# Performance work log

Measured on AMD Instinct MI355X. Metric: run time of the kernel, lower is better.

## Reference

```python
import jax, jax.numpy as jnp
import numpy as np

B, T, N, F = 8, 60, 400, 64
UNITS = 64
TIME_LEN = 12  # temporal conv kernel length
NEG = 1e16


def setup_inputs() -> dict:
    key = jax.random.key(0)
    ks = jax.random.split(key, 20)
    s = 0.05  # weight scale
    # sparse binary adjacency (k-hop support) with self-loops
    probs = jax.random.uniform(ks[0], (N, N))
    A = jnp.maximum((probs < 0.03).astype(jnp.float32), jnp.eye(N, dtype=jnp.float32))
    x = jax.random.normal(ks[1], (B, T, N, F), dtype=jnp.float32)
    inp = {
        'x': x,
        'A': A,
        # DynamicGC params
        'dgc_W1': jax.random.normal(ks[2], (N, N)) * s,
        'dgc_W2': jax.random.normal(ks[3], (F, N)) * s,
        'dgc_W3': jax.random.normal(ks[4], (F, UNITS)) * s,
        'dgc_b1': jax.random.normal(ks[5], (N,)) * s,
        'dgc_b2': jnp.zeros((UNITS,), jnp.float32),
        # TemporalAttention params (built on (T, N, UNITS))
        'ta_W1': jax.random.normal(ks[6], (N, 1)) * s,
        'ta_W2': jax.random.normal(ks[7], (UNITS, N)) * s,
        'ta_W3': jax.random.normal(ks[8], (UNITS, 1)) * s,
        'ta_Ve': jax.random.normal(ks[9], (T, T)) * s,
        'ta_be': jnp.zeros((T, T), jnp.float32),
        # temporal convs, kernel (TIME_LEN, 1), padding SAME, HWIO layout
        'tconv_k': jax.random.normal(ks[10], (TIME_LEN, 1, UNITS, UNITS)) * s,
        'tconv_b': jnp.zeros((UNITS,), jnp.float32),
        'rconv_k': jax.random.normal(ks[11], (TIME_LEN, 1, F, UNITS)) * s,
        'rconv_b': jnp.zeros((UNITS,), jnp.float32),
    }
    return inp


def _conv2d_same(x, k, b):
    # x: (B, T, N, Cin) NHWC, k: (TIME_LEN, 1, Cin, Cout) HWIO
    y = jax.lax.conv_general_dilated(
        x, k, window_strides=(1, 1), padding='SAME',
        dimension_numbers=('NHWC', 'HWIO', 'NHWC'))
    return y + b


def reference(x, A, dgc_W1, dgc_W2, dgc_W3, dgc_b1, dgc_b2,
              ta_W1, ta_W2, ta_W3, ta_Ve, ta_be,
              tconv_k, tconv_b, rconv_k, rconv_b):
    # ---- DynamicGC (TimeDistributed over T) ----
    AW = A * dgc_W1                                  # (N, N)
    # feature[b,t,m,f] = sum_n x[b,t,n,f] * AW[n,m]
    feat = jnp.einsum('btnf,nm->btmf', x, AW)
    dense = jnp.einsum('btmf,fj->btmj', feat, dgc_W2) + dgc_b1  # (B,T,N,N)
    logits = dense - NEG * (1.0 - A)
    attn = jax.nn.softmax(logits, axis=-1)           # (B,T,N,N)
    nodef = jnp.einsum('btmn,btnf->btmf', attn, x)   # (B,T,N,F)
    y = jnp.einsum('btnf,fu->btnu', nodef, dgc_W3) + dgc_b2  # (B,T,N,UNITS), linear activation

    # ---- TemporalAttention ----
    # lhs[b,t,n] = sum_f (sum_m y[b,t,m,f] * W1[m,0]) * W2[f,n]
    r1 = jnp.einsum('btnf,n->btf', y, ta_W1[:, 0])   # (B,T,UNITS)
    lhs = jnp.einsum('btf,fn->btn', r1, ta_W2)       # (B,T,N)
    rhs = jnp.einsum('btnf,f->btn', y, ta_W3[:, 0])  # (B,T,N), then transposed in contraction
    product = jnp.einsum('btn,bsn->bts', lhs, rhs)   # (B,T,T)
    E = jnp.einsum('jk,bkl->bjl', ta_Ve, jax.nn.sigmoid(product + ta_be))
    kernel = jax.nn.softmax(E, axis=-2)              # softmax over axis -2, (B,T,T)
    # conv[b,m,n,f] = sum_t y[b,t,n,f] * kernel[b,t,m]
    ta_out = jnp.einsum('btnf,btm->bmnf', y, kernel)  # (B,T,N,UNITS)

    # ---- temporal convs + residual + softplus ----
    tc = _conv2d_same(ta_out, tconv_k, tconv_b)
    res = _conv2d_same(x, rconv_k, rconv_b)
    return jax.nn.softplus(res + tc)
```

## Files before the change

kernel.cpp:

```cpp
#include <hip/hip_runtime.h>
#include <hip/hip_bf16.h>

typedef __attribute__((ext_vector_type(8))) short short8;
typedef __attribute__((ext_vector_type(4))) short short4_t;
typedef __attribute__((ext_vector_type(4))) float f32x4;

union P8u { unsigned char b[8]; long v; };

static __device__ __forceinline__ short f2b(float f) {
    union { float f; unsigned u; } v; v.f = f;
    unsigned r = v.u + 0x7FFFu + ((v.u >> 16) & 1u);
    return (short)(r >> 16);
}
static __device__ __forceinline__ unsigned char f2fp8(float f) {
    return (unsigned char)(__builtin_amdgcn_cvt_pk_fp8_f32(f, f, 0, false) & 0xff);
}

__global__ __launch_bounds__(256) void prep_w(
    const float* __restrict__ A, const float* __restrict__ W1,
    const float* __restrict__ W2, const float* __restrict__ W3,
    short* __restrict__ AWF, short* __restrict__ W2F,
    short* __restrict__ W3F, unsigned char* __restrict__ Ab2)
{
    int t = blockIdx.x * 256 + threadIdx.x;
    if (t < 422 * 64) {
        int tile = t >> 6, lane = t & 63, lm = lane & 15, quad = lane >> 4;
        short8 o;
        if (tile < 364) {
            int kt = tile % 13, g = tile / 13;
            int m = g * 16 + lm;
#pragma unroll
            for (int j = 0; j < 8; ++j) {
                int n = kt * 32 + quad * 8 + j;
                float v = (m < 400 && n < 400) ? A[n * 400 + m] * W1[n * 400 + m] : 0.f;
                o[j] = f2b(v);
            }
            *(short8*)(AWF + tile * 512 + lane * 8) = o;
        } else if (tile < 414) {
            int t2 = tile - 364;
            int kh = t2 & 1, jt = t2 >> 1;
            int jc = jt * 16 + lm;
#pragma unroll
            for (int j = 0; j < 8; ++j) {
                int f = kh * 32 + quad * 8 + j;
                o[j] = f2b(W2[f * 400 + jc]);
            }
            *(short8*)(W2F + t2 * 512 + lane * 8) = o;
        } else {
            int t3 = tile - 414;
            int kh = t3 & 1, ut = t3 >> 1;
            int u = ut * 16 + lm;
#pragma unroll
            for (int j = 0; j < 8; ++j) {
                int f = kh * 32 + quad * 8 + j;
                o[j] = f2b(W3[f * 64 + u]);
            }
            *(short8*)(W3F + t3 * 512 + lane * 8) = o;
        }
    } else {
        int o = t - 27008;
        if (o < 448 * 448) {
            int m = o / 448, j = o - m * 448;
            Ab2[o] = (m < 400 && j < 400 && A[m * 400 + j] != 0.f) ? 1 : 0;
        }
    }
}

__global__ __launch_bounds__(256) void prep_xt(
    const float* __restrict__ x, short* __restrict__ xF,
    unsigned char* __restrict__ xF8)
{
    int bt = blockIdx.x / 13, kt = blockIdx.x % 13;
    int tid = threadIdx.x, lane = tid & 63, ft = tid >> 6;
    int lm = lane & 15, quad = lane >> 4;
    const float* xs = x + (size_t)bt * 25600;
    int tile = kt * 4 + ft;
    int f = ft * 16 + lm;
    short8 ob; P8u p8;
#pragma unroll
    for (int j = 0; j < 8; ++j) {
        int n = kt * 32 + quad * 8 + j;
        float v = (n < 400) ? xs[(size_t)n * 64 + f] : 0.f;
        ob[j] = f2b(v);
        p8.b[j] = f2fp8(v);
    }
    size_t o = (size_t)bt * 26624 + tile * 512 + lane * 8;
    *(short8*)(xF + o) = ob;
    *(long*)(xF8 + o) = p8.v;
}

__global__ __launch_bounds__(64) void dgc_mfma(
    const float* __restrict__ b1p, const float* __restrict__ b2p,
    const unsigned* __restrict__ Ab2,
    const short* __restrict__ AWF, const short* __restrict__ W2F,
    const short* __restrict__ W3F, const short* __restrict__ xF,
    const unsigned char* __restrict__ xF8,
    const float* __restrict__ taW1, const float* __restrict__ taW3,
    short* __restrict__ y, float* __restrict__ rhs, float* __restrict__ r1)
{
    int bid = blockIdx.x;
    int c = bid & 7, jj = bid >> 3;
    int bt = c * 60 + jj / 14;
    int gg = jj % 14;
    int g0 = gg * 2;
    int lane = threadIdx.x;
    int lm = lane & 15, quad = lane >> 4;

    __shared__ __align__(16) char  attnS8[32 * 440];
    __shared__ __align__(16) short featS[32 * 72];
    __shared__ __align__(16) float invS[32];

    {
        *(long*)&attnS8[lm * 440 + 400 + quad * 8] = 0;
        *(long*)&attnS8[(16 + lm) * 440 + 400 + quad * 8] = 0;
        if (quad == 0) {
            *(long*)&attnS8[lm * 440 + 432] = 0;
            *(long*)&attnS8[(16 + lm) * 440 + 432] = 0;
        }
    }

    const short* xtb = xF + (size_t)bt * 26624 + lane * 8;
    const unsigned char* xt8b = xF8 + (size_t)bt * 26624 + lane * 8;

    f32x4 fa[2][4];
#pragma unroll
    for (int grp = 0; grp < 2; ++grp)
#pragma unroll
        for (int i = 0; i < 4; ++i) fa[grp][i] = (f32x4){0.f, 0.f, 0.f, 0.f};
    const short* awf0 = AWF + (size_t)g0 * 13 * 512 + lane * 8;
    const short* awf1 = awf0 + 13 * 512;
#pragma unroll
    for (int kb = 0; kb < 12; kb += 2) {
        short8 a00 = *(const short8*)(awf0 + kb * 512);
        short8 a01 = *(const short8*)(awf0 + (kb + 1) * 512);
        short8 a10 = *(const short8*)(awf1 + kb * 512);
        short8 a11 = *(const short8*)(awf1 + (kb + 1) * 512);
        short8 bf[8];
#pragma unroll
        for (int ft = 0; ft < 4; ++ft) {
            bf[ft]     = *(const short8*)(xtb + (kb * 4 + ft) * 512);
            bf[4 + ft] = *(const short8*)(xtb + ((kb + 1) * 4 + ft) * 512);
        }
#pragma unroll
        for (int ft = 0; ft < 4; ++ft) {
            fa[0][ft] = __builtin_amdgcn_mfma_f32_16x16x32_bf16(a00, bf[ft],     fa[0][ft], 0, 0, 0);
            fa[0][ft] = __builtin_amdgcn_mfma_f32_16x16x32_bf16(a01, bf[4 + ft], fa[0][ft], 0, 0, 0);
            fa[1][ft] = __builtin_amdgcn_mfma_f32_16x16x32_bf16(a10, bf[ft],     fa[1][ft], 0, 0, 0);
            fa[1][ft] = __builtin_amdgcn_mfma_f32_16x16x32_bf16(a11, bf[4 + ft], fa[1][ft], 0, 0, 0);
        }
    }
    {
        short8 a0t = *(const short8*)(awf0 + 12 * 512);
        short8 a1t = *(const short8*)(awf1 + 12 * 512);
        short8 bf[4];
#pragma unroll
        for (int ft = 0; ft < 4; ++ft)
            bf[ft] = *(const short8*)(xtb + (48 + ft) * 512);
#pragma unroll
        for (int ft = 0; ft < 4; ++ft) {
            fa[0][ft] = __builtin_amdgcn_mfma_f32_16x16x32_bf16(a0t, bf[ft], fa[0][ft], 0, 0, 0);
            fa[1][ft] = __builtin_amdgcn_mfma_f32_16x16x32_bf16(a1t, bf[ft], fa[1][ft], 0, 0, 0);
        }
    }
#pragma unroll
    for (int grp = 0; grp < 2; ++grp)
#pragma unroll
        for (int ft = 0; ft < 4; ++ft)
#pragma unroll
            for (int r = 0; r < 4; ++r)
                featS[(grp * 16 + quad * 4 + r) * 72 + ft * 16 + lm] = f2b(fa[grp][ft][r]);

    short8 a0g0 = *(const short8*)&featS[lm * 72 + quad * 8];
    short8 a1g0 = *(const short8*)&featS[lm * 72 + 32 + quad * 8];
    short8 a0g1 = *(const short8*)&featS[(16 + lm) * 72 + quad * 8];
    short8 a1g1 = *(const short8*)&featS[(16 + lm) * 72 + 32 + quad * 8];
    int m0 = g0 * 16 + lm;
    const unsigned* ab20 = Ab2 + (size_t)m0 * 112;
    const unsigned* ab21 = ab20 + 16 * 112;
    float s0 = 0.f, s1 = 0.f;
#pragma unroll
    for (int jb = 0; jb < 25; jb += 5) {
        short8 bf[10];
#pragma unroll
        for (int q = 0; q < 5; ++q) {
            bf[2 * q]     = *(const short8*)(W2F + ((jb + q) * 2 + 0) * 512 + lane * 8);
            bf[2 * q + 1] = *(const short8*)(W2F + ((jb + q) * 2 + 1) * 512 + lane * 8);
        }
        f32x4 d0[5], d1[5];
#pragma unroll
        for (int q = 0; q < 5; ++q) {
            d0[q] = (f32x4){0.f, 0.f, 0.f, 0.f};
            d0[q] = __builtin_amdgcn_mfma_f32_16x16x32_bf16(bf[2 * q],     a0g0, d0[q], 0, 0, 0);
            d0[q] = __builtin_amdgcn_mfma_f32_16x16x32_bf16(bf[2 * q + 1], a1g0, d0[q], 0, 0, 0);
            d1[q] = (f32x4){0.f, 0.f, 0.f, 0.f};
            d1[q] = __builtin_amdgcn_mfma_f32_16x16x32_bf16(bf[2 * q],     a0g1, d1[q], 0, 0, 0);
            d1[q] = __builtin_amdgcn_mfma_f32_16x16x32_bf16(bf[2 * q + 1], a1g1, d1[q], 0, 0, 0);
        }
#pragma unroll
        for (int q = 0; q < 5; ++q) {
            int jt = jb + q;
            float4 b1v = *(const float4*)(b1p + jt * 16 + quad * 4);
            {
                unsigned mv = ab20[jt * 4 + quad];
                float e0 = (mv & 255u)         ? __expf(d0[q][0] + b1v.x) : 0.f;
                float e1 = ((mv >> 8) & 255u)  ? __expf(d0[q][1] + b1v.y) : 0.f;
                float e2 = ((mv >> 16) & 255u) ? __expf(d0[q][2] + b1v.z) : 0.f;
                float e3 = ((mv >> 24) & 255u) ? __expf(d0[q][3] + b1v.w) : 0.f;
                s0 += (e0 + e1) + (e2 + e3);
                int pk = __builtin_amdgcn_cvt_pk_fp8_f32(e0, e1, 0, false);
                pk = __builtin_amdgcn_cvt_pk_fp8_f32(e2, e3, pk, true);
                *(int*)&attnS8[lm * 440 + jt * 16 + quad * 4] = pk;
            }
            {
                unsigned mv = ab21[jt * 4 + quad];
                float e0 = (mv & 255u)         ? __expf(d1[q][0] + b1v.x) : 0.f;
                float e1 = ((mv >> 8) & 255u)  ? __expf(d1[q][1] + b1v.y) : 0.f;
                float e2 = ((mv >> 16) & 255u) ? __expf(d1[q][2] + b1v.z) : 0.f;
                float e3 = ((mv >> 24) & 255u) ? __expf(d1[q][3] + b1v.w) : 0.f;
                s1 += (e0 + e1) + (e2 + e3);
                int pk = __builtin_amdgcn_cvt_pk_fp8_f32(e0, e1, 0, false);
                pk = __builtin_amdgcn_cvt_pk_fp8_f32(e2, e3, pk, true);
                *(int*)&attnS8[(16 + lm) * 440 + jt * 16 + quad * 4] = pk;
            }
        }
    }
    s0 += __shfl_xor(s0, 16);
    s0 += __shfl_xor(s0, 32);
    s1 += __shfl_xor(s1, 16);
    s1 += __shfl_xor(s1, 32);
    if (quad == 0) {
        invS[lm]      = (s0 > 0.f) ? (1.f / s0) : 0.f;
        invS[16 + lm] = (s1 > 0.f) ? (1.f / s1) : 0.f;
    }

    f32x4 na[2][4];
#pragma unroll
    for (int grp = 0; grp < 2; ++grp)
#pragma unroll
        for (int i = 0; i < 4; ++i) na[grp][i] = (f32x4){0.f, 0.f, 0.f, 0.f};
    const char* ar0 = attnS8 + lm * 440 + quad * 8;
    const char* ar1 = attnS8 + (16 + lm) * 440 + quad * 8;
#pragma unroll
    for (int kb = 0; kb < 12; kb += 2) {
        long f00 = *(const long*)(ar0 + kb * 32);
        long f01 = *(const long*)(ar0 + (kb + 1) * 32);
        long f10 = *(const long*)(ar1 + kb * 32);
        long f11 = *(const long*)(ar1 + (kb + 1) * 32);
        long bf[8];
#pragma unroll
        for (int ft = 0; ft < 4; ++ft) {
            bf[ft]     = *(const long*)(xt8b + (kb * 4 + ft) * 512);
            bf[4 + ft] = *(const long*)(xt8b + ((kb + 1) * 4 + ft) * 512);
        }
#pragma unroll
        for (int ft = 0; ft < 4; ++ft) {
            na[0][ft] = __builtin_amdgcn_mfma_f32_16x16x32_fp8_fp8(f00, bf[ft],     na[0][ft], 0, 0, 0);
            na[0][ft] = __builtin_amdgcn_mfma_f32_16x16x32_fp8_fp8(f01, bf[4 + ft], na[0][ft], 0, 0, 0);
            na[1][ft] = __builtin_amdgcn_mfma_f32_16x16x32_fp8_fp8(f10, bf[ft],     na[1][ft], 0, 0, 0);
            na[1][ft] = __builtin_amdgcn_mfma_f32_16x16x32_fp8_fp8(f11, bf[4 + ft], na[1][ft], 0, 0, 0);
        }
    }
    {
        long f0t = *(const long*)(ar0 + 12 * 32);
        long f1t = *(const long*)(ar1 + 12 * 32);
        long bf[4];
#pragma unroll
        for (int ft = 0; ft < 4; ++ft)
            bf[ft] = *(const long*)(xt8b + (48 + ft) * 512);
#pragma unroll
        for (int ft = 0; ft < 4; ++ft) {
            na[0][ft] = __builtin_amdgcn_mfma_f32_16x16x32_fp8_fp8(f0t, bf[ft], na[0][ft], 0, 0, 0);
            na[1][ft] = __builtin_amdgcn_mfma_f32_16x16x32_fp8_fp8(f1t, bf[ft], na[1][ft], 0, 0, 0);
        }
    }
#pragma unroll
    for (int grp = 0; grp < 2; ++grp)
#pragma unroll
        for (int ft = 0; ft < 4; ++ft)
#pragma unroll
            for (int r = 0; r < 4; ++r)
                featS[(grp * 16 + quad * 4 + r) * 72 + ft * 16 + lm] = f2b(na[grp][ft][r]);

    f32x4 ya[2][4];
#pragma unroll
    for (int grp = 0; grp < 2; ++grp)
#pragma unroll
        for (int i = 0; i < 4; ++i) ya[grp][i] = (f32x4){0.f, 0.f, 0.f, 0.f};
    short8 n00 = *(const short8*)&featS[lm * 72 + quad * 8];
    short8 n01 = *(const short8*)&featS[lm * 72 + 32 + quad * 8];
    short8 n10 = *(const short8*)&featS[(16 + lm) * 72 + quad * 8];
    short8 n11 = *(const short8*)&featS[(16 + lm) * 72 + 32 + quad * 8];
    {
        short8 wb[8];
#pragma unroll
        for (int ut = 0; ut < 4; ++ut) {
            wb[2 * ut]     = *(const short8*)(W3F + (ut * 2 + 0) * 512 + lane * 8);
            wb[2 * ut + 1] = *(const short8*)(W3F + (ut * 2 + 1) * 512 + lane * 8);
        }
#pragma unroll
        for (int ut = 0; ut < 4; ++ut) {
            ya[0][ut] = __builtin_amdgcn_mfma_f32_16x16x32_bf16(n00, wb[2 * ut],     ya[0][ut], 0, 0, 0);
            ya[0][ut] = __builtin_amdgcn_mfma_f32_16x16x32_bf16(n01, wb[2 * ut + 1], ya[0][ut], 0, 0, 0);
            ya[1][ut] = __builtin_amdgcn_mfma_f32_16x16x32_bf16(n10, wb[2 * ut],     ya[1][ut], 0, 0, 0);
            ya[1][ut] = __builtin_amdgcn_mfma_f32_16x16x32_bf16(n11, wb[2 * ut + 1], ya[1][ut], 0, 0, 0);
        }
    }

    float w3r[4];
#pragma unroll
    for (int ut = 0; ut < 4; ++ut) w3r[ut] = taW3[ut * 16 + lm];
#pragma unroll
    for (int grp = 0; grp < 2; ++grp) {
        int mrb = (g0 + grp) * 16 + quad * 4;
        float4 inv4 = *(const float4*)&invS[grp * 16 + quad * 4];
        float invr[4] = {inv4.x, inv4.y, inv4.z, inv4.w};
        float yv[4][4];
#pragma unroll
        for (int ut = 0; ut < 4; ++ut) {
            int u = ut * 16 + lm;
            float b2v = b2p[u];
#pragma unroll
            for (int r = 0; r < 4; ++r) {
                yv[ut][r] = ya[grp][ut][r] * invr[r] + b2v;
                int mrow = mrb + r;
                if (mrow < 400)
                    y[((size_t)bt * 400 + mrow) * 64 + u] = f2b(yv[ut][r]);
            }
        }
        float rv[4];
#pragma unroll
        for (int r = 0; r < 4; ++r) {
            float v = yv[0][r] * w3r[0] + yv[1][r] * w3r[1] +
                      yv[2][r] * w3r[2] + yv[3][r] * w3r[3];
            v += __shfl_xor(v, 1);
            v += __shfl_xor(v, 2);
            v += __shfl_xor(v, 4);
            v += __shfl_xor(v, 8);
            rv[r] = v;
        }
        if (lm == 0 && mrb < 400)
            *(float4*)(rhs + (size_t)bt * 400 + mrb) = make_float4(rv[0], rv[1], rv[2], rv[3]);
        float p[4] = {0.f, 0.f, 0.f, 0.f};
#pragma unroll
        for (int r = 0; r < 4; ++r) {
            int mrow = mrb + r;
            if (mrow < 400) {
                float w1v = taW1[mrow];
#pragma unroll
                for (int ut = 0; ut < 4; ++ut) p[ut] += yv[ut][r] * w1v;
            }
        }
#pragma unroll
        for (int ut = 0; ut < 4; ++ut) {
            p[ut] += __shfl_xor(p[ut], 16);
            p[ut] += __shfl_xor(p[ut], 32);
        }
        if (quad == 0) {
#pragma unroll
            for (int ut = 0; ut < 4; ++ut)
                atomicAdd(&r1[bt * 64 + ut * 16 + lm], p[ut]);
        }
    }
}

__global__ __launch_bounds__(256) void ta_lhs(
    const float* __restrict__ r1, const float* __restrict__ taW2,
    float* __restrict__ lhs)
{
    int bt = blockIdx.x, tid = threadIdx.x;
    __shared__ float r1s[64];
    if (tid < 64) r1s[tid] = r1[bt * 64 + tid];
    __syncthreads();
    for (int n = tid; n < 400; n += 256) {
        float acc = 0.f;
#pragma unroll 8
        for (int f = 0; f < 64; ++f) acc += r1s[f] * taW2[f * 400 + n];
        lhs[bt * 400 + n] = acc;
    }
}

__global__ __launch_bounds__(256) void ta_product(
    const float* __restrict__ lhs, const float* __restrict__ rhs,
    const float* __restrict__ be, float* __restrict__ S)
{
    int kc = blockIdx.x, b = blockIdx.y, tid = threadIdx.x;
    if (tid >= 240) return;
    int k = kc * 4 + tid / 60;
    int l = tid % 60;
    const float4* lr = (const float4*)(lhs + (size_t)(b * 60 + k) * 400);
    const float4* rr = (const float4*)(rhs + (size_t)(b * 60 + l) * 400);
    float acc = 0.f;
    for (int q = 0; q < 100; ++q) {
        float4 a = lr[q], c = rr[q];
        acc += a.x * c.x + a.y * c.y + a.z * c.z + a.w * c.w;
    }
    float v = acc + be[k * 60 + l];
    S[b * 3600 + k * 60 + l] = 1.f / (1.f + __expf(-v));
}

__global__ __launch_bounds__(256) void ta_softmax(
    const float* __restrict__ S, const float* __restrict__ Ve,
    float* __restrict__ ker)
{
    int b = blockIdx.x, tid = threadIdx.x;
    __shared__ float Ss[3600];
    __shared__ float Emat[3600];
    for (int i = tid; i < 3600; i += 256) Ss[i] = S[b * 3600 + i];
    __syncthreads();
    for (int p = tid; p < 3600; p += 256) {
        int j = p / 60, l = p % 60;
        float acc = 0.f;
        for (int k = 0; k < 60; ++k) acc += Ve[j * 60 + k] * Ss[k * 60 + l];
        Emat[p] = acc;
    }
    __syncthreads();
    for (int l = tid; l < 60; l += 256) {
        float mx = -1e30f;
        for (int j = 0; j < 60; ++j) mx = fmaxf(mx, Emat[j * 60 + l]);
        float s = 0.f;
        for (int j = 0; j < 60; ++j) s += __expf(Emat[j * 60 + l] - mx);
        float inv = 1.f / s;
        for (int j = 0; j < 60; ++j)
            ker[b * 3600 + j * 60 + l] = __expf(Emat[j * 60 + l] - mx) * inv;
    }
}

__global__ __launch_bounds__(256) void ktf_prep(
    const float* __restrict__ tk, const float* __restrict__ rk,
    short* __restrict__ KTF)
{
    int i = blockIdx.x * 256 + threadIdx.x;
    int j = i & 7, lane = (i >> 3) & 63, tile = i >> 9;
    int kkt = tile % 48, ng = tile / 48;
    int u = (ng >> 1) * 32 + (ng & 1) * 16 + (lane & 15);
    int kk = kkt * 32 + (lane >> 4) * 8 + j;
    int dt = kk >> 7, c = kk & 127;
    float v = (c < 64) ? tk[dt * 4096 + c * 64 + u]
                       : rk[dt * 4096 + (c - 64) * 64 + u];
    KTF[i] = f2b(v);
}

#define IN_S 136
__global__ __launch_bounds__(256, 4) void fused_conv(
    const short* __restrict__ y, const float* __restrict__ ker,
    const float* __restrict__ x, const short* __restrict__ KTF,
    const float* __restrict__ tb, const float* __restrict__ rb,
    float* __restrict__ out)
{
    int n = blockIdx.x, b = blockIdx.y;
    int tid = threadIdx.x, lane = tid & 63, w = tid >> 6;
    int m = lane & 15, quad = lane >> 4;
    int hm = w >> 1, hn = w & 1;

    __shared__ __align__(16) short In[75 * IN_S];
    __shared__ __align__(16) short kerT[64 * 72];
    __shared__ __align__(16) short ybT[64 * 72];

    {
        for (int i = tid; i < 1020; i += 256) {
            int o = (i < 340) ? i : i + 4080;
            ((int*)In)[o] = 0;
        }
        int4 z4; z4.x = 0; z4.y = 0; z4.z = 0; z4.w = 0;
        for (int i = tid; i < 576; i += 256) {
            ((int4*)kerT)[i] = z4;
            ((int4*)ybT)[i] = z4;
        }
    }
    __syncthreads();

    for (int i = tid; i < 960; i += 256) {
        int t = i >> 4, uq = (i & 15) * 4;
        float4 xv = *(const float4*)&x[((size_t)(b * 60 + t) * 400 + n) * 64 + uq];
        short4_t o;
        o[0] = f2b(xv.x); o[1] = f2b(xv.y); o[2] = f2b(xv.z); o[3] = f2b(xv.w);
        *(short4_t*)&In[(t + 5) * IN_S + 64 + uq] = o;
    }
    for (int i = tid; i < 960; i += 256) {
        int s = i >> 4, uq = (i & 15) * 4;
        short4_t yv = *(const short4_t*)&y[((size_t)(b * 60 + s) * 400 + n) * 64 + uq];
#pragma unroll
        for (int k = 0; k < 4; ++k) ybT[(uq + k) * 72 + s] = yv[k];
    }
    for (int i = tid; i < 900; i += 256) {
        int s = i / 15, t4 = (i % 15) * 4;
        float4 kv = *(const float4*)&ker[b * 3600 + s * 60 + t4];
        kerT[(t4 + 0) * 72 + s] = f2b(kv.x);
        kerT[(t4 + 1) * 72 + s] = f2b(kv.y);
        kerT[(t4 + 2) * 72 + s] = f2b(kv.z);
        kerT[(t4 + 3) * 72 + s] = f2b(kv.w);
    }
    __syncthreads();

    f32x4 tacc[2][2];
#pragma unroll
    for (int a = 0; a < 2; ++a)
#pragma unroll
        for (int c = 0; c < 2; ++c) tacc[a][c] = (f32x4){0.f, 0.f, 0.f, 0.f};
#pragma unroll
    for (int k0 = 0; k0 < 64; k0 += 32) {
        short8 afr[2], bfr[2];
#pragma unroll
        for (int mt = 0; mt < 2; ++mt)
            afr[mt] = *(const short8*)&kerT[(hm * 32 + mt * 16 + m) * 72 + k0 + quad * 8];
#pragma unroll
        for (int nt = 0; nt < 2; ++nt)
            bfr[nt] = *(const short8*)&ybT[(hn * 32 + nt * 16 + m) * 72 + k0 + quad * 8];
#pragma unroll
        for (int mt = 0; mt < 2; ++mt)
#pragma unroll
            for (int nt = 0; nt < 2; ++nt)
                tacc[mt][nt] = __builtin_amdgcn_mfma_f32_16x16x32_bf16(
                    afr[mt], bfr[nt], tacc[mt][nt], 0, 0, 0);
    }
    __syncthreads();

#pragma unroll
    for (int mt = 0; mt < 2; ++mt)
#pragma unroll
        for (int nt = 0; nt < 2; ++nt)
#pragma unroll
            for (int r = 0; r < 4; ++r) {
                int t = hm * 32 + mt * 16 + quad * 4 + r;
                int u = hn * 32 + nt * 16 + m;
                if (t < 60) In[(t + 5) * IN_S + u] = f2b(tacc[mt][nt][r]);
            }
    __syncthreads();

    f32x4 acc[2][2];
#pragma unroll
    for (int a = 0; a < 2; ++a)
#pragma unroll
        for (int c = 0; c < 2; ++c) acc[a][c] = (f32x4){0.f, 0.f, 0.f, 0.f};

    const short* ktf0 = KTF + (size_t)(hn * 2 + 0) * 48 * 512 + lane * 8;
    const short* ktf1 = KTF + (size_t)(hn * 2 + 1) * 48 * 512 + lane * 8;

#pragma unroll 4
    for (int kb = 0; kb < 48; kb += 2) {
        short8 a0[2], a1[2];
        short8 b0[2], b1[2];
#pragma unroll
        for (int q = 0; q < 2; ++q) {
            int kk = (kb + q) * 32;
            int dt = kk >> 7, c0 = (kk & 127) + quad * 8;
            int i0 = (hm * 32 + m + dt) * IN_S + c0;
            a0[q] = *(const short8*)&In[i0];
            a1[q] = *(const short8*)&In[i0 + 16 * IN_S];
            b0[q] = *(const short8*)(ktf0 + (kb + q) * 512);
            b1[q] = *(const short8*)(ktf1 + (kb + q) * 512);
        }
#pragma unroll
        for (int q = 0; q < 2; ++q) {
            acc[0][0] = __builtin_amdgcn_mfma_f32_16x16x32_bf16(a0[q], b0[q], acc[0][0], 0, 0, 0);
            acc[0][1] = __builtin_amdgcn_mfma_f32_16x16x32_bf16(a0[q], b1[q], acc[0][1], 0, 0, 0);
            acc[1][0] = __builtin_amdgcn_mfma_f32_16x16x32_bf16(a1[q], b0[q], acc[1][0], 0, 0, 0);
            acc[1][1] = __builtin_amdgcn_mfma_f32_16x16x32_bf16(a1[q], b1[q], acc[1][1], 0, 0, 0);
        }
    }

    float bias[2];
#pragma unroll
    for (int nt = 0; nt < 2; ++nt) {
        int u = hn * 32 + nt * 16 + m;
        bias[nt] = tb[u] + rb[u];
    }
#pragma unroll
    for (int mt = 0; mt < 2; ++mt)
#pragma unroll
        for (int r = 0; r < 4; ++r) {
            int t = hm * 32 + mt * 16 + quad * 4 + r;
            if (t >= 60) continue;
#pragma unroll
            for (int nt = 0; nt < 2; ++nt) {
                int u = hn * 32 + nt * 16 + m;
                float v = acc[mt][nt][r] + bias[nt];
                float e = __expf(-fabsf(v));
                float sp = fmaxf(v, 0.f) + __logf(1.f + e);
                out[((size_t)(b * 60 + t) * 400 + n) * 64 + u] = sp;
            }
        }
}

extern "C" void kernel_launch(void* const* d_in, const int* in_sizes, int n_in,
                              void* d_out, int out_size, void* d_ws, size_t ws_size,
                              hipStream_t stream)
{
    const float* x    = (const float*)d_in[0];
    const float* A    = (const float*)d_in[1];
    const float* W1   = (const float*)d_in[2];
    const float* W2   = (const float*)d_in[3];
    const float* W3   = (const float*)d_in[4];
    const float* b1   = (const float*)d_in[5];
    const float* b2   = (const float*)d_in[6];
    const float* taW1 = (const float*)d_in[7];
    const float* taW2 = (const float*)d_in[8];
    const float* taW3 = (const float*)d_in[9];
    const float* Ve   = (const float*)d_in[10];
    const float* be   = (const float*)d_in[11];
    const float* tk   = (const float*)d_in[12];
    const float* tb   = (const float*)d_in[13];
    const float* rk   = (const float*)d_in[14];
    const float* rb   = (const float*)d_in[15];
    float* out = (float*)d_out;

    char* wsb = (char*)d_ws;
    size_t off = 0;
    auto alloc = [&](size_t bytes) -> void* {
        void* p = wsb + off;
        off += (bytes + 255) & ~(size_t)255;
        return p;
    };
    short* AWF           = (short*)alloc((size_t)186368 * 2);
    short* W2F           = (short*)alloc((size_t)25600 * 2);
    short* W3F           = (short*)alloc((size_t)4096 * 2);
    unsigned char* Ab2   = (unsigned char*)alloc((size_t)448 * 448);
    short* xF            = (short*)alloc((size_t)480 * 26624 * 2);
    unsigned char* xF8   = (unsigned char*)alloc((size_t)480 * 26624);
    short* y             = (short*)alloc((size_t)480 * 400 * 64 * 2);
    float* r1            = (float*)alloc(480 * 64 * 4);
    float* rhs           = (float*)alloc(480 * 400 * 4);
    float* lhs           = (float*)alloc(480 * 400 * 4);
    float* Sbuf          = (float*)alloc(8 * 3600 * 4);
    float* ker           = (float*)alloc(8 * 3600 * 4);
    short* KTF           = (short*)alloc((size_t)98304 * 2);

    hipMemsetAsync(r1, 0, 480 * 64 * 4, stream);
    prep_w<<<890, 256, 0, stream>>>(A, W1, W2, W3, AWF, W2F, W3F, Ab2);
    prep_xt<<<6240, 256, 0, stream>>>(x, xF, xF8);
    dgc_mfma<<<6720, 64, 0, stream>>>(b1, b2, (const unsigned*)Ab2,
                                      AWF, W2F, W3F, xF, xF8,
                                      taW1, taW3, y, rhs, r1);
    ta_lhs<<<480, 256, 0, stream>>>(r1, taW2, lhs);
    ta_product<<<dim3(15, 8), 256, 0, stream>>>(lhs, rhs, be, Sbuf);
    ta_softmax<<<8, 256, 0, stream>>>(Sbuf, Ve, ker);
    ktf_prep<<<384, 256, 0, stream>>>(tk, rk, KTF);
    fused_conv<<<dim3(400, 8), 256, 0, stream>>>(y, ker, x, KTF, tb, rb, out);
}
```

Baseline: 343.7 us.

## Stream attention chunks through double-buffered LDS, fusing exp with attn×x MFMA

```diff
diff --git a/kernel.cpp b/kernel.cpp
--- a/kernel.cpp
+++ b/kernel.cpp
@@ -14,6 +14,19 @@
 }
 static __device__ __forceinline__ unsigned char f2fp8(float f) {
     return (unsigned char)(__builtin_amdgcn_cvt_pk_fp8_f32(f, f, 0, false) & 0xff);
+}
+
+static __device__ __forceinline__ float bemit(
+    f32x4 d, float4 b1v, unsigned mv, char* dst)
+{
+    float e0 = (mv & 255u)         ? __expf(d[0] + b1v.x) : 0.f;
+    float e1 = ((mv >> 8) & 255u)  ? __expf(d[1] + b1v.y) : 0.f;
+    float e2 = ((mv >> 16) & 255u) ? __expf(d[2] + b1v.z) : 0.f;
+    float e3 = ((mv >> 24) & 255u) ? __expf(d[3] + b1v.w) : 0.f;
+    int pk = __builtin_amdgcn_cvt_pk_fp8_f32(e0, e1, 0, false);
+    pk = __builtin_amdgcn_cvt_pk_fp8_f32(e2, e3, pk, true);
+    *(int*)dst = pk;
+    return (e0 + e1) + (e2 + e3);
 }
 
 __global__ __launch_bounds__(256) void prep_w(
@@ -89,6 +102,7 @@
     *(long*)(xF8 + o) = p8.v;
 }
 
+#define CBS 1280
 __global__ __launch_bounds__(64) void dgc_mfma(
     const float* __restrict__ b1p, const float* __restrict__ b2p,
     const unsigned* __restrict__ Ab2,
@@ -106,18 +120,9 @@
     int lane = threadIdx.x;
     int lm = lane & 15, quad = lane >> 4;
 
-    __shared__ __align__(16) char  attnS8[32 * 440];
     __shared__ __align__(16) short featS[32 * 72];
+    __shared__ __align__(16) char  chunkS[2 * CBS];
     __shared__ __align__(16) float invS[32];
-
-    {
-        *(long*)&attnS8[lm * 440 + 400 + quad * 8] = 0;
-        *(long*)&attnS8[(16 + lm) * 440 + 400 + quad * 8] = 0;
-        if (quad == 0) {
-            *(long*)&attnS8[lm * 440 + 432] = 0;
-            *(long*)&attnS8[(16 + lm) * 440 + 432] = 0;
-        }
-    }
 
     const short* xtb = xF + (size_t)bt * 26624 + lane * 8;
     const unsigned char* xt8b = xF8 + (size_t)bt * 26624 + lane * 8;
@@ -178,52 +183,75 @@
     const unsigned* ab20 = Ab2 + (size_t)m0 * 112;
     const unsigned* ab21 = ab20 + 16 * 112;
     float s0 = 0.f, s1 = 0.f;
-#pragma unroll
-    for (int jb = 0; jb < 25; jb += 5) {
-        short8 bf[10];
-#pragma unroll
-        for (int q = 0; q < 5; ++q) {
-            bf[2 * q]     = *(const short8*)(W2F + ((jb + q) * 2 + 0) * 512 + lane * 8);
-            bf[2 * q + 1] = *(const short8*)(W2F + ((jb + q) * 2 + 1) * 512 + lane * 8);
-        }
-        f32x4 d0[5], d1[5];
-#pragma unroll
-        for (int q = 0; q < 5; ++q) {
-            d0[q] = (f32x4){0.f, 0.f, 0.f, 0.f};
-            d0[q] = __builtin_amdgcn_mfma_f32_16x16x32_bf16(bf[2 * q],     a0g0, d0[q], 0, 0, 0);
-            d0[q] = __builtin_amdgcn_mfma_f32_16x16x32_bf16(bf[2 * q + 1], a1g0, d0[q], 0, 0, 0);
-            d1[q] = (f32x4){0.f, 0.f, 0.f, 0.f};
-            d1[q] = __builtin_amdgcn_mfma_f32_16x16x32_bf16(bf[2 * q],     a0g1, d1[q], 0, 0, 0);
-            d1[q] = __builtin_amdgcn_mfma_f32_16x16x32_bf16(bf[2 * q + 1], a1g1, d1[q], 0, 0, 0);
-        }
-#pragma unroll
-        for (int q = 0; q < 5; ++q) {
-            int jt = jb + q;
-            float4 b1v = *(const float4*)(b1p + jt * 16 + quad * 4);
-            {
-                unsigned mv = ab20[jt * 4 + quad];
-                float e0 = (mv & 255u)         ? __expf(d0[q][0] + b1v.x) : 0.f;
-                float e1 = ((mv >> 8) & 255u)  ? __expf(d0[q][1] + b1v.y) : 0.f;
-                float e2 = ((mv >> 16) & 255u) ? __expf(d0[q][2] + b1v.z) : 0.f;
-                float e3 = ((mv >> 24) & 255u) ? __expf(d0[q][3] + b1v.w) : 0.f;
-                s0 += (e0 + e1) + (e2 + e3);
-                int pk = __builtin_amdgcn_cvt_pk_fp8_f32(e0, e1, 0, false);
-                pk = __builtin_amdgcn_cvt_pk_fp8_f32(e2, e3, pk, true);
-                *(int*)&attnS8[lm * 440 + jt * 16 + quad * 4] = pk;
-            }
-            {
-                unsigned mv = ab21[jt * 4 + quad];
-                float e0 = (mv & 255u)         ? __expf(d1[q][0] + b1v.x) : 0.f;
-                float e1 = ((mv >> 8) & 255u)  ? __expf(d1[q][1] + b1v.y) : 0.f;
-                float e2 = ((mv >> 16) & 255u) ? __expf(d1[q][2] + b1v.z) : 0.f;
-                float e3 = ((mv >> 24) & 255u) ? __expf(d1[q][3] + b1v.w) : 0.f;
-                s1 += (e0 + e1) + (e2 + e3);
-                int pk = __builtin_amdgcn_cvt_pk_fp8_f32(e0, e1, 0, false);
-                pk = __builtin_amdgcn_cvt_pk_fp8_f32(e2, e3, pk, true);
-                *(int*)&attnS8[(16 + lm) * 440 + jt * 16 + quad * 4] = pk;
-            }
-        }
-    }
+    f32x4 na[2][4];
+#pragma unroll
+    for (int grp = 0; grp < 2; ++grp)
+#pragma unroll
+        for (int i = 0; i < 4; ++i) na[grp][i] = (f32x4){0.f, 0.f, 0.f, 0.f};
+    char* row0 = chunkS + lm * 40;
+    char* row1 = chunkS + (16 + lm) * 40;
+
+#define BCHUNK(cc)                                                             \
+    {                                                                          \
+        char* cb0 = row0 + ((cc) & 1) * CBS;                                   \
+        char* cb1 = row1 + ((cc) & 1) * CBS;                                   \
+        int jt0 = 2 * (cc);                                                    \
+        const short* wp = W2F + (size_t)jt0 * 1024 + lane * 8;                 \
+        float4 bv0 = *(const float4*)(b1p + jt0 * 16 + quad * 4);              \
+        short8 w0 = *(const short8*)(wp);                                      \
+        short8 w1 = *(const short8*)(wp + 512);                                \
+        f32x4 d;                                                               \
+        d = (f32x4){0.f, 0.f, 0.f, 0.f};                                       \
+        d = __builtin_amdgcn_mfma_f32_16x16x32_bf16(w0, a0g0, d, 0, 0, 0);     \
+        d = __builtin_amdgcn_mfma_f32_16x16x32_bf16(w1, a1g0, d, 0, 0, 0);     \
+        s0 += bemit(d, bv0, ab20[jt0 * 4 + quad], cb0 + quad * 4);             \
+        d = (f32x4){0.f, 0.f, 0.f, 0.f};                                       \
+        d = __builtin_amdgcn_mfma_f32_16x16x32_bf16(w0, a0g1, d, 0, 0, 0);     \
+        d = __builtin_amdgcn_mfma_f32_16x16x32_bf16(w1, a1g1, d, 0, 0, 0);     \
+        s1 += bemit(d, bv0, ab21[jt0 * 4 + quad], cb1 + quad * 4);             \
+        if ((cc) < 12) {                                                       \
+            float4 bv1 = *(const float4*)(b1p + (jt0 + 1) * 16 + quad * 4);    \
+            short8 w2 = *(const short8*)(wp + 1024);                           \
+            short8 w3 = *(const short8*)(wp + 1536);                           \
+            d = (f32x4){0.f, 0.f, 0.f, 0.f};                                   \
+            d = __builtin_amdgcn_mfma_f32_16x16x32_bf16(w2, a0g0, d, 0, 0, 0); \
+            d = __builtin_amdgcn_mfma_f32_16x16x32_bf16(w3, a1g0, d, 0, 0, 0); \
+            s0 += bemit(d, bv1, ab20[jt0 * 4 + 4 + quad], cb0 + 16 + quad * 4);\
+            d = (f32x4){0.f, 0.f, 0.f, 0.f};                                   \
+            d = __builtin_amdgcn_mfma_f32_16x16x32_bf16(w2, a0g1, d, 0, 0, 0); \
+            d = __builtin_amdgcn_mfma_f32_16x16x32_bf16(w3, a1g1, d, 0, 0, 0); \
+            s1 += bemit(d, bv1, ab21[jt0 * 4 + 4 + quad], cb1 + 16 + quad * 4);\
+        } else {                                                               \
+            *(int*)(cb0 + 16 + quad * 4) = 0;              \
+            *(int*)(cb1 + 16 + quad * 4) = 0;                                  \
+        }                                                                      \
+    }
+
+    BCHUNK(0)
+#pragma unroll
+    for (int ck = 0; ck < 13; ++ck) {
+        asm volatile("" ::: "memory");
+        if (ck < 12) BCHUNK(ck + 1)
+        const char* cb0 = row0 + (ck & 1) * CBS;
+        const char* cb1 = row1 + (ck & 1) * CBS;
+        int lo0 = *(const int*)(cb0 + quad * 8);
+        int hi0 = *(const int*)(cb0 + quad * 8 + 4);
+        int lo1 = *(const int*)(cb1 + quad * 8);
+        int hi1 = *(const int*)(cb1 + quad * 8 + 4);
+        long afg0 = (long)(((unsigned long long)(unsigned)hi0 << 32) | (unsigned)lo0);
+        long afg1 = (long)(((unsigned long long)(unsigned)hi1 << 32) | (unsigned)lo1);
+        long bf[4];
+#pragma unroll
+        for (int ft = 0; ft < 4; ++ft)
+            bf[ft] = *(const long*)(xt8b + (ck * 4 + ft) * 512);
+#pragma unroll
+        for (int ft = 0; ft < 4; ++ft) {
+            na[0][ft] = __builtin_amdgcn_mfma_f32_16x16x32_fp8_fp8(afg0, bf[ft], na[0][ft], 0, 0, 0);
+            na[1][ft] = __builtin_amdgcn_mfma_f32_16x16x32_fp8_fp8(afg1, bf[ft], na[1][ft], 0, 0, 0);
+        }
+    }
+#undef BCHUNK
+
     s0 += __shfl_xor(s0, 16);
     s0 += __shfl_xor(s0, 32);
     s1 += __shfl_xor(s1, 16);
@@ -231,47 +259,6 @@
     if (quad == 0) {
         invS[lm]      = (s0 > 0.f) ? (1.f / s0) : 0.f;
         invS[16 + lm] = (s1 > 0.f) ? (1.f / s1) : 0.f;
-    }
-
-    f32x4 na[2][4];
-#pragma unroll
-    for (int grp = 0; grp < 2; ++grp)
-#pragma unroll
-        for (int i = 0; i < 4; ++i) na[grp][i] = (f32x4){0.f, 0.f, 0.f, 0.f};
-    const char* ar0 = attnS8 + lm * 440 + quad * 8;
-    const char* ar1 = attnS8 + (16 + lm) * 440 + quad * 8;
-#pragma unroll
-    for (int kb = 0; kb < 12; kb += 2) {
-        long f00 = *(const long*)(ar0 + kb * 32);
-        long f01 = *(const long*)(ar0 + (kb + 1) * 32);
-        long f10 = *(const long*)(ar1 + kb * 32);
-        long f11 = *(const long*)(ar1 + (kb + 1) * 32);
-        long bf[8];
-#pragma unroll
-        for (int ft = 0; ft < 4; ++ft) {
-            bf[ft]     = *(const long*)(xt8b + (kb * 4 + ft) * 512);
-            bf[4 + ft] = *(const long*)(xt8b + ((kb + 1) * 4 + ft) * 512);
-        }
-#pragma unroll
-        for (int ft = 0; ft < 4; ++ft) {
-            na[0][ft] = __builtin_amdgcn_mfma_f32_16x16x32_fp8_fp8(f00, bf[ft],     na[0][ft], 0, 0, 0);
-            na[0][ft] = __builtin_amdgcn_mfma_f32_16x16x32_fp8_fp8(f01, bf[4 + ft], na[0][ft], 0, 0, 0);
-            na[1][ft] = __builtin_amdgcn_mfma_f32_16x16x32_fp8_fp8(f10, bf[ft],     na[1][ft], 0, 0, 0);
-            na[1][ft] = __builtin_amdgcn_mfma_f32_16x16x32_fp8_fp8(f11, bf[4 + ft], na[1][ft], 0, 0, 0);
-        }
-    }
-    {
-        long f0t = *(const long*)(ar0 + 12 * 32);
-        long f1t = *(const long*)(ar1 + 12 * 32);
-        long bf[4];
-#pragma unroll
-        for (int ft = 0; ft < 4; ++ft)
-            bf[ft] = *(const long*)(xt8b + (48 + ft) * 512);
-#pragma unroll
-        for (int ft = 0; ft < 4; ++ft) {
-            na[0][ft] = __builtin_amdgcn_mfma_f32_16x16x32_fp8_fp8(f0t, bf[ft], na[0][ft], 0, 0, 0);
-            na[1][ft] = __builtin_amdgcn_mfma_f32_16x16x32_fp8_fp8(f1t, bf[ft], na[1][ft], 0, 0, 0);
-        }
     }
 #pragma unroll
     for (int grp = 0; grp < 2; ++grp)
```

Measured after the change: 344.5 us. Within noise of the previous version (+0.2%).
